# Kernel tuning notes

Hardware: AMD Instinct MI355X
Metric: run time of the kernel (lower is better)

Reference implementation:

```python
import jax, jax.numpy as jnp
import numpy as np
from jax import lax

EPS = 1e-5
HEADS = 8

def _proj(x, i, w1, b1, g1, be1, m1, v1, w2, b2, g2, be2, m2, v2):
    # Conv2d(1,8,3,1,1) -> BN(8) -> ReLU -> Conv2d(8,1,3,1,1) -> BN(1) -> ReLU (eval-mode BN)
    dn = ('NCHW', 'OIHW', 'NCHW')
    def bn(y, g, b, m, v):
        return g[None, :, None, None] * (y - m[None, :, None, None]) * lax.rsqrt(v + EPS)[None, :, None, None] + b[None, :, None, None]
    y = lax.conv_general_dilated(x, w1[i], (1, 1), 'SAME', dimension_numbers=dn) + b1[i][None, :, None, None]
    y = jax.nn.relu(bn(y, g1[i], be1[i], m1[i], v1[i]))
    y = lax.conv_general_dilated(y, w2[i], (1, 1), 'SAME', dimension_numbers=dn) + b2[i][None, :, None, None]
    return jax.nn.relu(bn(y, g2[i], be2[i], m2[i], v2[i]))

def setup_inputs() -> dict:
    key = jax.random.key(0)
    ks = jax.random.split(key, 4)
    B, L, D = 4, 512, 512
    X = jax.random.normal(ks[0], (B, L, D), dtype=jnp.float32)
    valid_lens = jax.random.randint(ks[1], (B,), 1, L + 1, dtype=jnp.int32)
    # stacked params for the 4 projection blocks: 0=Q, 1=K, 2=V, 3=out
    w1 = jax.random.normal(ks[2], (4, 8, 1, 3, 3), dtype=jnp.float32) * 0.2
    w2 = jax.random.normal(ks[3], (4, 1, 8, 3, 3), dtype=jnp.float32) * 0.2
    b1 = jnp.zeros((4, 8), jnp.float32); b2 = jnp.zeros((4, 1), jnp.float32)
    g1 = jnp.ones((4, 8), jnp.float32);  g2 = jnp.ones((4, 1), jnp.float32)
    be1 = jnp.zeros((4, 8), jnp.float32); be2 = jnp.zeros((4, 1), jnp.float32)
    m1 = jnp.zeros((4, 8), jnp.float32);  m2 = jnp.zeros((4, 1), jnp.float32)
    v1 = jnp.ones((4, 8), jnp.float32);   v2 = jnp.ones((4, 1), jnp.float32)
    return {"X": X, "valid_lens": valid_lens, "w1": w1, "b1": b1, "g1": g1, "be1": be1,
            "m1": m1, "v1": v1, "w2": w2, "b2": b2, "g2": g2, "be2": be2, "m2": m2, "v2": v2}

def reference(X, valid_lens, w1, b1, g1, be1, m1, v1, w2, b2, g2, be2, m2, v2):
    B, L, D = X.shape
    H = HEADS
    d = D // H
    p = (w1, b1, g1, be1, m1, v1, w2, b2, g2, be2, m2, v2)
    X4 = X[:, None]  # [B,1,L,D]
    Q = _proj(X4, 0, *p)
    K = _proj(X4, 1, *p)
    V = _proj(X4, 2, *p)
    def split(Y):  # [B,1,L,D] -> [B,H,L,d]
        return Y.reshape(B, L, H, d).transpose(0, 2, 1, 3)
    q, k, v = split(Q), split(K), split(V)
    # cross-head scores: score[b,i,j,m,n] = <q[b,i,m], k[b,j,n]> / sqrt(d)
    score = jnp.einsum('bimd,bjnd->bijmn', q, k) / jnp.sqrt(jnp.float32(d))
    attn = jax.nn.softmax(score, axis=-1)  # [B,H,H,L,L]
    # context[b,i,m] = sum_j attn[b,i,j] @ v[b,j]  (sum over second head axis)
    ctx = jnp.einsum('bijmn,bjnd->bimd', attn, v)  # [B,H,L,d]
    ctx = ctx.transpose(0, 2, 1, 3).reshape(B, L, D)
    out = _proj(ctx[:, None], 3, *p).reshape(B, L, D)
    return out, attn
```

## Files before the change

### kernel.cpp

```cpp
#include <hip/hip_runtime.h>


typedef __bf16 bf16x8 __attribute__((ext_vector_type(8)));
typedef float  f32x4  __attribute__((ext_vector_type(4)));

__global__ __launch_bounds__(256)
void conv_proj_kernel(const float* __restrict__ in, int nparts,
                      float* __restrict__ out, int fixed_proj,
                      const float* __restrict__ w1, const float* __restrict__ b1,
                      const float* __restrict__ g1, const float* __restrict__ be1,
                      const float* __restrict__ m1, const float* __restrict__ v1,
                      const float* __restrict__ w2, const float* __restrict__ b2,
                      const float* __restrict__ g2, const float* __restrict__ be2,
                      const float* __restrict__ m2, const float* __restrict__ v2,
                      ushort* __restrict__ vth, ushort* __restrict__ vtl)
{
  __shared__ float xs[36][36];
  __shared__ float ys[8][34][34];
  __shared__ float w1s[8][9];
  __shared__ float w2s[8][9];
  __shared__ float a1s[8], c1s[8];
  __shared__ float a2s[1], c2s[1];

  const int t = threadIdx.x;
  int proj, b;
  if (fixed_proj < 0) { proj = blockIdx.z >> 2; b = blockIdx.z & 3; }
  else                { proj = fixed_proj;      b = blockIdx.z;     }
  const int h0 = blockIdx.y * 32;
  const int w0 = blockIdx.x * 32;

  if (t < 72) {
    w1s[t / 9][t % 9] = w1[proj * 72 + t];
    w2s[t / 9][t % 9] = w2[proj * 72 + t];
  } else if (t < 80) {
    int ch = t - 72;
    float a = g1[proj * 8 + ch] * rsqrtf(v1[proj * 8 + ch] + 1e-5f);
    a1s[ch] = a;
    c1s[ch] = fmaf(a, b1[proj * 8 + ch] - m1[proj * 8 + ch], be1[proj * 8 + ch]);
  } else if (t == 80) {
    float a = g2[proj] * rsqrtf(v2[proj] + 1e-5f);
    a2s[0] = a;
    c2s[0] = fmaf(a, b2[proj] - m2[proj], be2[proj]);
  }

  for (int idx = t; idx < 36 * 36; idx += 256) {
    int r = idx / 36, c = idx - r * 36;
    int hg = h0 - 2 + r, wg = w0 - 2 + c;
    float val = 0.f;
    if (hg >= 0 && hg < 512 && wg >= 0 && wg < 512) {
      int off = b * 262144 + hg * 512 + wg;
      if (nparts == 1) {
        val = in[off];
      } else {
        #pragma unroll
        for (int p = 0; p < 8; ++p) val += in[p * 1048576 + off];
      }
    }
    xs[r][c] = val;
  }
  __syncthreads();

  for (int idx = t; idx < 34 * 34; idx += 256) {
    int r = idx / 34, c = idx - r * 34;
    int hg1 = h0 - 1 + r, wg1 = w0 - 1 + c;
    bool inside = (hg1 >= 0) & (hg1 < 512) & (wg1 >= 0) & (wg1 < 512);
    float x0 = xs[r    ][c], x1 = xs[r    ][c + 1], x2 = xs[r    ][c + 2];
    float x3 = xs[r + 1][c], x4 = xs[r + 1][c + 1], x5 = xs[r + 1][c + 2];
    float x6 = xs[r + 2][c], x7 = xs[r + 2][c + 1], x8 = xs[r + 2][c + 2];
    #pragma unroll
    for (int ch = 0; ch < 8; ++ch) {
      const float* w = w1s[ch];
      float acc = w[0] * x0 + w[1] * x1 + w[2] * x2
                + w[3] * x3 + w[4] * x4 + w[5] * x5
                + w[6] * x6 + w[7] * x7 + w[8] * x8;
      float y = fmaxf(fmaf(acc, a1s[ch], c1s[ch]), 0.f);
      ys[ch][r][c] = inside ? y : 0.f;
    }
  }
  __syncthreads();

  const int r0 = (t >> 4) * 2;
  const int c0 = (t & 15) * 2;
  float o00 = 0.f, o01 = 0.f, o10 = 0.f, o11 = 0.f;
  #pragma unroll
  for (int ch = 0; ch < 8; ++ch) {
    float win[4][4];
    #pragma unroll
    for (int rr = 0; rr < 4; ++rr) {
      float2 p0 = *(const float2*)&ys[ch][r0 + rr][c0];
      float2 p1 = *(const float2*)&ys[ch][r0 + rr][c0 + 2];
      win[rr][0] = p0.x; win[rr][1] = p0.y; win[rr][2] = p1.x; win[rr][3] = p1.y;
    }
    #pragma unroll
    for (int dh = 0; dh < 3; ++dh)
      #pragma unroll
      for (int dw = 0; dw < 3; ++dw) {
        float wgt = w2s[ch][dh * 3 + dw];
        o00 = fmaf(wgt, win[dh    ][dw    ], o00);
        o01 = fmaf(wgt, win[dh    ][dw + 1], o01);
        o10 = fmaf(wgt, win[dh + 1][dw    ], o10);
        o11 = fmaf(wgt, win[dh + 1][dw + 1], o11);
      }
  }
  const float a2 = a2s[0], cc2 = c2s[0];
  float v00 = fmaxf(fmaf(o00, a2, cc2), 0.f);
  float v01 = fmaxf(fmaf(o01, a2, cc2), 0.f);
  float v10 = fmaxf(fmaf(o10, a2, cc2), 0.f);
  float v11 = fmaxf(fmaf(o11, a2, cc2), 0.f);

  const bool is_v = (fixed_proj < 0) && (proj == 2);
  if (!is_v) {
    const int sel = (fixed_proj < 0) ? proj : 0;
    float* ob = out + sel * 1048576 + b * 262144;
    *(float2*)&ob[(h0 + r0    ) * 512 + (w0 + c0)] = make_float2(v00, v01);
    *(float2*)&ob[(h0 + r0 + 1) * 512 + (w0 + c0)] = make_float2(v10, v11);
  } else {
    float* xf = &xs[0][0];
    xf[(r0    ) * 33 + c0    ] = v00;
    xf[(r0    ) * 33 + c0 + 1] = v01;
    xf[(r0 + 1) * 33 + c0    ] = v10;
    xf[(r0 + 1) * 33 + c0 + 1] = v11;
    __syncthreads();
    const int dl = t >> 3;
    const int ll = (t & 7) * 4;
    uint hb[4], lb[4];
    #pragma unroll
    for (int k = 0; k < 4; ++k) {
      float x = xf[(ll + k) * 33 + dl];
      uint u = __float_as_uint(x);
      hb[k] = u >> 16;
      float r = x - __uint_as_float(u & 0xFFFF0000u);
      lb[k] = __float_as_uint(r) >> 16;
    }
    uint2 hv = make_uint2(hb[0] | (hb[1] << 16), hb[2] | (hb[3] << 16));
    uint2 lv = make_uint2(lb[0] | (lb[1] << 16), lb[2] | (lb[3] << 16));
    size_t off = (size_t)b * 262144 + (size_t)(w0 + dl) * 512 + (h0 + ll);
    *(uint2*)(vth + off) = hv;
    *(uint2*)(vtl + off) = lv;
  }
}

__global__ __launch_bounds__(256)
void attn_fused_kernel(const float* __restrict__ Q, const float* __restrict__ K,
                       const ushort* __restrict__ vth, const ushort* __restrict__ vtl,
                       float* __restrict__ attn, float* __restrict__ ctxp)
{
  __shared__ __align__(16) float smem[12288];
  float* qs = smem;
  float* kt = smem + 2176;
  ushort* Ph = (ushort*)smem;
  ushort* Pl = (ushort*)(smem + 2048);
  ushort* Vh = (ushort*)(smem + 4096);
  ushort* Vl = (ushort*)(smem + 8192);

  const int t  = threadIdx.x;
  const int b  = blockIdx.z;
  const int ij = blockIdx.y;
  const int i  = ij >> 3, j = ij & 7;
  const int m0 = blockIdx.x * 32;

  const int tm = t >> 5;
  const int tn = t & 31;

  {
    int m = t >> 3, d0 = (t & 7) * 8;
    const float* qp = &Q[b * 262144 + (m0 + m) * 512 + i * 64 + d0];
    float4 qa = *(const float4*)qp;
    float4 qb = *(const float4*)(qp + 4);
    *(float4*)&qs[m * 68 + d0] =
        make_float4(qa.x * 0.125f, qa.y * 0.125f, qa.z * 0.125f, qa.w * 0.125f);
    *(float4*)&qs[m * 68 + d0 + 4] =
        make_float4(qb.x * 0.125f, qb.y * 0.125f, qb.z * 0.125f, qb.w * 0.125f);
  }

  float S[4][4][4];

  #pragma unroll
  for (int c = 0; c < 4; ++c) {
    __syncthreads();
    {
      int n = t >> 1, d0 = (t & 1) * 32;
      const float* kp = &K[b * 262144 + (c * 128 + n) * 512 + j * 64 + d0];
      #pragma unroll
      for (int q4 = 0; q4 < 8; ++q4) {
        float4 kv = *(const float4*)&kp[q4 * 4];
        kt[(d0 + q4 * 4 + 0) * 132 + n] = kv.x;
        kt[(d0 + q4 * 4 + 1) * 132 + n] = kv.y;
        kt[(d0 + q4 * 4 + 2) * 132 + n] = kv.z;
        kt[(d0 + q4 * 4 + 3) * 132 + n] = kv.w;
      }
    }
    __syncthreads();
    #pragma unroll
    for (int mm = 0; mm < 4; ++mm)
      #pragma unroll
      for (int nn = 0; nn < 4; ++nn) S[c][mm][nn] = 0.f;
    #pragma unroll 2
    for (int dd = 0; dd < 64; dd += 4) {
      float4 k0 = *(const float4*)&kt[(dd + 0) * 132 + tn * 4];
      float4 k1 = *(const float4*)&kt[(dd + 1) * 132 + tn * 4];
      float4 k2 = *(const float4*)&kt[(dd + 2) * 132 + tn * 4];
      float4 k3 = *(const float4*)&kt[(dd + 3) * 132 + tn * 4];
      #pragma unroll
      for (int mm = 0; mm < 4; ++mm) {
        float4 qv = *(const float4*)&qs[(tm + 8 * mm) * 68 + dd];
        S[c][mm][0] = fmaf(qv.x, k0.x, fmaf(qv.y, k1.x, fmaf(qv.z, k2.x, fmaf(qv.w, k3.x, S[c][mm][0]))));
        S[c][mm][1] = fmaf(qv.x, k0.y, fmaf(qv.y, k1.y, fmaf(qv.z, k2.y, fmaf(qv.w, k3.y, S[c][mm][1]))));
        S[c][mm][2] = fmaf(qv.x, k0.z, fmaf(qv.y, k1.z, fmaf(qv.z, k2.z, fmaf(qv.w, k3.z, S[c][mm][2]))));
        S[c][mm][3] = fmaf(qv.x, k0.w, fmaf(qv.y, k1.w, fmaf(qv.z, k2.w, fmaf(qv.w, k3.w, S[c][mm][3]))));
      }
    }
  }

  float* ap = attn + (size_t)((b * 8 + i) * 8 + j) * 262144;
  #pragma unroll
  for (int mm = 0; mm < 4; ++mm) {
    float mx = -3.0e38f;
    #pragma unroll
    for (int c = 0; c < 4; ++c)
      #pragma unroll
      for (int nn = 0; nn < 4; ++nn) mx = fmaxf(mx, S[c][mm][nn]);
    #pragma unroll
    for (int off = 1; off < 32; off <<= 1) mx = fmaxf(mx, __shfl_xor(mx, off));
    float sum = 0.f;
    #pragma unroll
    for (int c = 0; c < 4; ++c)
      #pragma unroll
      for (int nn = 0; nn < 4; ++nn) {
        float e = __expf(S[c][mm][nn] - mx);
        S[c][mm][nn] = e;
        sum += e;
      }
    #pragma unroll
    for (int off = 1; off < 32; off <<= 1) sum += __shfl_xor(sum, off);
    float rinv = 1.0f / sum;
    float* rowp = ap + (size_t)(m0 + tm + 8 * mm) * 512;
    #pragma unroll
    for (int c = 0; c < 4; ++c) {
      float4 o = make_float4(S[c][mm][0] * rinv, S[c][mm][1] * rinv,
                             S[c][mm][2] * rinv, S[c][mm][3] * rinv);
      S[c][mm][0] = o.x; S[c][mm][1] = o.y; S[c][mm][2] = o.z; S[c][mm][3] = o.w;
      *(float4*)&rowp[c * 128 + tn * 4] = o;
    }
  }

  const int lane = t & 63;
  const int w    = t >> 6;
  const int q0   = (w & 1) * 16;
  const int d0   = (w >> 1) * 32;
  const int frow = lane & 15;
  const int kgrp = lane >> 4;
  f32x4 acc0 = {0.f, 0.f, 0.f, 0.f};
  f32x4 acc1 = {0.f, 0.f, 0.f, 0.f};

  const ushort* vhg = vth + (size_t)b * 262144 + (size_t)(j * 64) * 512;
  const ushort* vlg = vtl + (size_t)b * 262144 + (size_t)(j * 64) * 512;

  for (int c = 0; c < 4; ++c) {
    __syncthreads();
    #pragma unroll
    for (int mm = 0; mm < 4; ++mm) {
      int row = tm + 8 * mm;
      uint hb[4], lb[4];
      #pragma unroll
      for (int nn = 0; nn < 4; ++nn) {
        float x = S[c][mm][nn];
        uint u = __float_as_uint(x);
        hb[nn] = u >> 16;
        float r = x - __uint_as_float(u & 0xFFFF0000u);
        lb[nn] = __float_as_uint(r) >> 16;
      }
      uint2 hv = make_uint2(hb[0] | (hb[1] << 16), hb[2] | (hb[3] << 16));
      uint2 lv = make_uint2(lb[0] | (lb[1] << 16), lb[2] | (lb[3] << 16));
      int bo = (row * 256 + tn * 8) ^ ((row & 7) << 4);
      *(uint2*)((char*)Ph + bo) = hv;
      *(uint2*)((char*)Pl + bo) = lv;
    }
    {
      int d = t >> 2, l0 = (t & 3) * 32;
      const ushort* sh = vhg + (size_t)d * 512 + c * 128 + l0;
      const ushort* sl = vlg + (size_t)d * 512 + c * 128 + l0;
      #pragma unroll
      for (int q = 0; q < 4; ++q) {
        uint4 hv4 = *(const uint4*)(sh + q * 8);
        uint4 lv4 = *(const uint4*)(sl + q * 8);
        int bo = (d * 256 + l0 * 2 + q * 16) ^ ((d & 7) << 4);
        *(uint4*)((char*)Vh + bo) = hv4;
        *(uint4*)((char*)Vl + bo) = lv4;
      }
    }
    __syncthreads();
    #pragma unroll
    for (int ks = 0; ks < 4; ++ks) {
      int ka = ks * 64 + kgrp * 16;
      int ao  = ((q0 + frow) * 256 + ka) ^ ((frow & 7) << 4);
      int bo0 = ((d0 + frow) * 256 + ka) ^ ((frow & 7) << 4);
      int bo1 = ((d0 + 16 + frow) * 256 + ka) ^ ((frow & 7) << 4);
      bf16x8 ah  = __builtin_bit_cast(bf16x8, *(const uint4*)((const char*)Ph + ao));
      bf16x8 al  = __builtin_bit_cast(bf16x8, *(const uint4*)((const char*)Pl + ao));
      bf16x8 bh0 = __builtin_bit_cast(bf16x8, *(const uint4*)((const char*)Vh + bo0));
      bf16x8 bl0 = __builtin_bit_cast(bf16x8, *(const uint4*)((const char*)Vl + bo0));
      bf16x8 bh1 = __builtin_bit_cast(bf16x8, *(const uint4*)((const char*)Vh + bo1));
      bf16x8 bl1 = __builtin_bit_cast(bf16x8, *(const uint4*)((const char*)Vl + bo1));
      acc0 = __builtin_amdgcn_mfma_f32_16x16x32_bf16(ah, bh0, acc0, 0, 0, 0);
      acc1 = __builtin_amdgcn_mfma_f32_16x16x32_bf16(ah, bh1, acc1, 0, 0, 0);
      acc0 = __builtin_amdgcn_mfma_f32_16x16x32_bf16(ah, bl0, acc0, 0, 0, 0);
      acc1 = __builtin_amdgcn_mfma_f32_16x16x32_bf16(ah, bl1, acc1, 0, 0, 0);
      acc0 = __builtin_amdgcn_mfma_f32_16x16x32_bf16(al, bh0, acc0, 0, 0, 0);
      acc1 = __builtin_amdgcn_mfma_f32_16x16x32_bf16(al, bh1, acc1, 0, 0, 0);
    }
  }

  float* op = ctxp + j * 1048576 + b * 262144 + i * 64;
  const int qbase = m0 + q0 + kgrp * 4;
  #pragma unroll
  for (int r = 0; r < 4; ++r) {
    op[(size_t)(qbase + r) * 512 + d0 + frow]      = acc0[r];
    op[(size_t)(qbase + r) * 512 + d0 + 16 + frow] = acc1[r];
  }
}

extern "C" void kernel_launch(void* const* d_in, const int* in_sizes, int n_in,
                              void* d_out, int out_size, void* d_ws, size_t ws_size,
                              hipStream_t stream)
{
  const float* X   = (const float*)d_in[0];
  const float* w1  = (const float*)d_in[2];
  const float* b1  = (const float*)d_in[3];
  const float* g1  = (const float*)d_in[4];
  const float* be1 = (const float*)d_in[5];
  const float* m1  = (const float*)d_in[6];
  const float* v1  = (const float*)d_in[7];
  const float* w2  = (const float*)d_in[8];
  const float* b2  = (const float*)d_in[9];
  const float* g2  = (const float*)d_in[10];
  const float* be2 = (const float*)d_in[11];
  const float* m2  = (const float*)d_in[12];
  const float* v2  = (const float*)d_in[13];

  float* ws   = (float*)d_ws;
  float* Qb   = ws;
  float* Kb   = ws + 1048576;
  ushort* Vth = (ushort*)(ws + 2097152);
  ushort* Vtl = (ushort*)(ws + 2621440);
  float* ctxp = ws + 3145728;
  float* outp = (float*)d_out;
  float* attn = outp + 1048576;

  conv_proj_kernel<<<dim3(16, 16, 12), 256, 0, stream>>>(
      X, 1, ws, -1, w1, b1, g1, be1, m1, v1, w2, b2, g2, be2, m2, v2, Vth, Vtl);

  attn_fused_kernel<<<dim3(16, 64, 4), 256, 0, stream>>>(Qb, Kb, Vth, Vtl, attn, ctxp);

  conv_proj_kernel<<<dim3(16, 16, 4), 256, 0, stream>>>(
      ctxp, 8, outp, 3, w1, b1, g1, be1, m1, v1, w2, b2, g2, be2, m2, v2,
      nullptr, nullptr);
}
```

Before: 469.8 us.

## Fuse three kernels into one persistent cooperative kernel with grid syncs

Replaces the three launches (QKV conv projection, fused attention, output conv projection) with a single persistent cooperative kernel. Stages are separated by grid.sync, and the attention and output stages pull tiles from atomic work counters. The goal is to remove launch overhead and inter-kernel gaps and to balance load dynamically. In exchange it pays grid-wide barrier costs, caps occupancy at 3 blocks per CU through a union of the shared-memory buffers, and resets the counters in a way that could race with the atomics.

Result: slower. 789.7 us (+68.1%).

```diff
diff --git a/kernel.cpp b/kernel.cpp
--- a/kernel.cpp
+++ b/kernel.cpp
@@ -1,33 +1,58 @@
 #include <hip/hip_runtime.h>
+#include <hip/hip_cooperative_groups.h>
+
+namespace cg = cooperative_groups;
 
 
 typedef __bf16 bf16x8 __attribute__((ext_vector_type(8)));
 typedef float  f32x4  __attribute__((ext_vector_type(4)));
 
-__global__ __launch_bounds__(256)
-void conv_proj_kernel(const float* __restrict__ in, int nparts,
-                      float* __restrict__ out, int fixed_proj,
-                      const float* __restrict__ w1, const float* __restrict__ b1,
-                      const float* __restrict__ g1, const float* __restrict__ be1,
-                      const float* __restrict__ m1, const float* __restrict__ v1,
-                      const float* __restrict__ w2, const float* __restrict__ b2,
-                      const float* __restrict__ g2, const float* __restrict__ be2,
-                      const float* __restrict__ m2, const float* __restrict__ v2,
-                      ushort* __restrict__ vth, ushort* __restrict__ vtl)
+struct ConvSmem {
+  float xs[36][36];
+  float ys[8][34][34];
+  float w1s[8][9];
+  float w2s[8][9];
+  float a1s[8], c1s[8];
+  float a2s[1], c2s[1];
+};
+
+struct MegaSmem {
+  union {
+    ConvSmem conv;
+    float attn[12288];
+  };
+};
+
+__device__ int g_cntB = 0;
+__device__ int g_cntC = 0;
+
+__device__ __forceinline__ void conv_body(
+    const float* __restrict__ in, int nparts, float* __restrict__ out,
+    int fixed_proj,
+    const float* __restrict__ w1, const float* __restrict__ b1,
+    const float* __restrict__ g1, const float* __restrict__ be1,
+    const float* __restrict__ m1, const float* __restrict__ v1,
+    const float* __restrict__ w2, const float* __restrict__ b2,
+    const float* __restrict__ g2, const float* __restrict__ be2,
+    const float* __restrict__ m2, const float* __restrict__ v2,
+    ushort* __restrict__ vth, ushort* __restrict__ vtl,
+    int bx, int by, int bz, ConvSmem& sm)
 {
-  __shared__ float xs[36][36];
-  __shared__ float ys[8][34][34];
-  __shared__ float w1s[8][9];
-  __shared__ float w2s[8][9];
-  __shared__ float a1s[8], c1s[8];
-  __shared__ float a2s[1], c2s[1];
+  auto& xs  = sm.xs;
+  auto& ys  = sm.ys;
+  auto& w1s = sm.w1s;
+  auto& w2s = sm.w2s;
+  auto& a1s = sm.a1s;
+  auto& c1s = sm.c1s;
+  auto& a2s = sm.a2s;
+  auto& c2s = sm.c2s;
 
   const int t = threadIdx.x;
   int proj, b;
-  if (fixed_proj < 0) { proj = blockIdx.z >> 2; b = blockIdx.z & 3; }
-  else                { proj = fixed_proj;      b = blockIdx.z;     }
-  const int h0 = blockIdx.y * 32;
-  const int w0 = blockIdx.x * 32;
+  if (fixed_proj < 0) { proj = bz >> 2; b = bz & 3; }
+  else                { proj = fixed_proj; b = bz;  }
+  const int h0 = by * 32;
+  const int w0 = bx * 32;
 
   if (t < 72) {
     w1s[t / 9][t % 9] = w1[proj * 72 + t];
@@ -140,12 +165,12 @@
   }
 }
 
-__global__ __launch_bounds__(256)
-void attn_fused_kernel(const float* __restrict__ Q, const float* __restrict__ K,
-                       const ushort* __restrict__ vth, const ushort* __restrict__ vtl,
-                       float* __restrict__ attn, float* __restrict__ ctxp)
+__device__ __forceinline__ void attn_body(
+    const float* __restrict__ Q, const float* __restrict__ K,
+    const ushort* __restrict__ vth, const ushort* __restrict__ vtl,
+    float* __restrict__ attnp, float* __restrict__ ctxp,
+    int bx, int by, int bz, float* smem)
 {
-  __shared__ __align__(16) float smem[12288];
   float* qs = smem;
   float* kt = smem + 2176;
   ushort* Ph = (ushort*)smem;
@@ -154,10 +179,10 @@
   ushort* Vl = (ushort*)(smem + 8192);
 
   const int t  = threadIdx.x;
-  const int b  = blockIdx.z;
-  const int ij = blockIdx.y;
+  const int b  = bz;
+  const int ij = by;
   const int i  = ij >> 3, j = ij & 7;
-  const int m0 = blockIdx.x * 32;
+  const int m0 = bx * 32;
 
   const int tm = t >> 5;
   const int tn = t & 31;
@@ -212,7 +237,7 @@
     }
   }
 
-  float* ap = attn + (size_t)((b * 8 + i) * 8 + j) * 262144;
+  float* ap = attnp + (size_t)((b * 8 + i) * 8 + j) * 262144;
   #pragma unroll
   for (int mm = 0; mm < 4; ++mm) {
     float mx = -3.0e38f;
@@ -320,6 +345,58 @@
   }
 }
 
+__global__ __launch_bounds__(256, 3)
+void mega_kernel(const float* __restrict__ X,
+                 const float* __restrict__ w1, const float* __restrict__ b1,
+                 const float* __restrict__ g1, const float* __restrict__ be1,
+                 const float* __restrict__ m1, const float* __restrict__ v1,
+                 const float* __restrict__ w2, const float* __restrict__ b2,
+                 const float* __restrict__ g2, const float* __restrict__ be2,
+                 const float* __restrict__ m2, const float* __restrict__ v2,
+                 float* __restrict__ ws, float* __restrict__ outp)
+{
+  __shared__ MegaSmem sm;
+  __shared__ int s_task;
+  cg::grid_group grid = cg::this_grid();
+
+  float*  Qb   = ws;
+  float*  Kb   = ws + 1048576;
+  ushort* Vth  = (ushort*)(ws + 2097152);
+  ushort* Vtl  = (ushort*)(ws + 2621440);
+  float*  ctxp = ws + 3145728;
+  float*  attnp = outp + 1048576;
+
+  if (blockIdx.x == 0 && threadIdx.x == 0) { g_cntB = 0; g_cntC = 0; }
+
+  for (int task = blockIdx.x; task < 3072; task += gridDim.x) {
+    __syncthreads();
+    conv_body(X, 1, ws, -1, w1, b1, g1, be1, m1, v1, w2, b2, g2, be2, m2, v2,
+              Vth, Vtl, task & 15, (task >> 4) & 15, task >> 8, sm.conv);
+  }
+
+  grid.sync();
+
+  for (;;) {
+    if (threadIdx.x == 0) s_task = atomicAdd(&g_cntB, 1);
+    __syncthreads();
+    int task = s_task;
+    if (task >= 4096) break;
+    attn_body(Qb, Kb, Vth, Vtl, attnp, ctxp,
+              task & 15, (task >> 4) & 63, task >> 10, sm.attn);
+  }
+
+  grid.sync();
+
+  for (;;) {
+    if (threadIdx.x == 0) s_task = atomicAdd(&g_cntC, 1);
+    __syncthreads();
+    int task = s_task;
+    if (task >= 1024) break;
+    conv_body(ctxp, 8, outp, 3, w1, b1, g1, be1, m1, v1, w2, b2, g2, be2, m2, v2,
+              nullptr, nullptr, task & 15, (task >> 4) & 15, task >> 8, sm.conv);
+  }
+}
+
 extern "C" void kernel_launch(void* const* d_in, const int* in_sizes, int n_in,
                               void* d_out, int out_size, void* d_ws, size_t ws_size,
                               hipStream_t stream)
@@ -337,22 +414,23 @@
   const float* be2 = (const float*)d_in[11];
   const float* m2  = (const float*)d_in[12];
   const float* v2  = (const float*)d_in[13];
-
   float* ws   = (float*)d_ws;
-  float* Qb   = ws;
-  float* Kb   = ws + 1048576;
-  ushort* Vth = (ushort*)(ws + 2097152);
-  ushort* Vtl = (ushort*)(ws + 2621440);
-  float* ctxp = ws + 3145728;
   float* outp = (float*)d_out;
-  float* attn = outp + 1048576;
-
-  conv_proj_kernel<<<dim3(16, 16, 12), 256, 0, stream>>>(
-      X, 1, ws, -1, w1, b1, g1, be1, m1, v1, w2, b2, g2, be2, m2, v2, Vth, Vtl);
-
-  attn_fused_kernel<<<dim3(16, 64, 4), 256, 0, stream>>>(Qb, Kb, Vth, Vtl, attn, ctxp);
-
-  conv_proj_kernel<<<dim3(16, 16, 4), 256, 0, stream>>>(
-      ctxp, 8, outp, 3, w1, b1, g1, be1, m1, v1, w2, b2, g2, be2, m2, v2,
-      nullptr, nullptr);
+
+  static int bpc = 0;
+  if (bpc == 0) {
+    int n = 0;
+    hipError_t e = hipOccupancyMaxActiveBlocksPerMultiprocessor(
+        &n, mega_kernel, 256, 0);
+    bpc = (e == hipSuccess && n >= 1) ? (n > 3 ? 3 : n) : 2;
+  }
+  dim3 gridDim(256 * bpc);
+  dim3 blockDim(256);
+
+  void* args[] = {
+      (void*)&X,  (void*)&w1, (void*)&b1,  (void*)&g1, (void*)&be1,
+      (void*)&m1, (void*)&v1, (void*)&w2,  (void*)&b2, (void*)&g2,
+      (void*)&be2,(void*)&m2, (void*)&v2,  (void*)&ws, (void*)&outp };
+
+  hipLaunchCooperativeKernel(mega_kernel, gridDim, blockDim, args, 0, stream);
 }
```
